# Kernel tuning notes

Hardware: AMD Instinct MI355X
Metric: run time of the kernel (lower is better)

## Reference

```python
import jax, jax.numpy as jnp
import numpy as np

DIMS = 1024
HEAD = 16
HEAD_DIM = DIMS // HEAD  # 64
BASE_THETA = 10000.0


def setup_inputs() -> dict:
    key = jax.random.key(0)
    ks = jax.random.split(key, 8)
    B, S = 2, 2048
    x = jax.random.normal(ks[0], (B, S, DIMS), dtype=jnp.float32)
    # causal additive mask (use -1e9 instead of -inf for finite grads)
    mask = jnp.where(jnp.tril(jnp.ones((S, S), dtype=bool)), 0.0, -1e9).astype(jnp.float32)
    init = 0.02
    Wq = jax.random.normal(ks[1], (DIMS, DIMS), dtype=jnp.float32) * init
    bq = jnp.zeros((DIMS,), dtype=jnp.float32)
    Wk = jax.random.normal(ks[2], (DIMS, DIMS), dtype=jnp.float32) * init  # no bias
    Wv = jax.random.normal(ks[3], (DIMS, DIMS), dtype=jnp.float32) * init
    bv = jnp.zeros((DIMS,), dtype=jnp.float32)
    Wo = jax.random.normal(ks[4], (DIMS, DIMS), dtype=jnp.float32) * init
    bo = jnp.zeros((DIMS,), dtype=jnp.float32)
    # learned rotary frequencies, initialized exactly as the torch module
    inv_freq = (1.0 / (BASE_THETA ** (jnp.arange(0, HEAD_DIM, 2, dtype=jnp.float32) / HEAD_DIM))).astype(jnp.float32)
    return {"x": x, "mask": mask, "Wq": Wq, "bq": bq, "Wk": Wk, "Wv": Wv,
            "bv": bv, "Wo": Wo, "bo": bo, "inv_freq": inv_freq}


def _apply_rotary(x, cos, sin):
    # x: [B,H,S,D] with D == 2 * len(inv_freq); cos/sin: [S, D/2]
    xr = x.reshape(*x.shape[:-1], -1, 2)  # [B,H,S,D/2,2]
    a, b = xr[..., 0], xr[..., 1]
    ra = a * cos - b * sin
    rb = a * sin + b * cos
    return jnp.stack([ra, rb], axis=-1).reshape(x.shape)


def reference(x, mask, Wq, bq, Wk, Wv, bv, Wo, bo, inv_freq):
    B, S, D = x.shape
    H, hd = HEAD, HEAD_DIM
    q = jnp.einsum('bsd,ed->bse', x, Wq) + bq
    k = jnp.einsum('bsd,ed->bse', x, Wk)
    v = jnp.einsum('bsd,ed->bse', x, Wv) + bv
    # [B,S,D] -> [B,H,S,hd]
    q = q.reshape(B, S, H, hd).transpose(0, 2, 1, 3)
    k = k.reshape(B, S, H, hd).transpose(0, 2, 1, 3)
    v = v.reshape(B, S, H, hd).transpose(0, 2, 1, 3)
    # rotary embeddings (complex mul expressed with cos/sin)
    t = jnp.arange(S, dtype=jnp.float32)
    freqs = t[:, None] * inv_freq[None, :]  # [S, hd/2]
    cos, sin = jnp.cos(freqs), jnp.sin(freqs)
    q = _apply_rotary(q, cos, sin)
    k = _apply_rotary(k, cos, sin)
    scale = hd ** (-0.25)
    qk = jnp.einsum('bhqd,bhkd->bhqk', q * scale, k * scale)
    qk = qk + mask[:S, :S]
    qk = qk.astype(jnp.float32)
    w = jax.nn.softmax(qk, axis=-1)  # dropout is identity in eval mode
    out = jnp.einsum('bhqk,bhkd->bhqd', w, v)
    out = out.transpose(0, 2, 1, 3).reshape(B, S, D)
    out = jnp.einsum('bsd,ed->bse', out, Wo) + bo
    return (out, qk)
```

## Files before the change

### kernel.cpp

```cpp
#include <hip/hip_runtime.h>

typedef __attribute__((ext_vector_type(8))) short short8;
typedef __attribute__((ext_vector_type(4))) float floatx4;
typedef unsigned short ushort_t;

typedef __attribute__((address_space(1))) const ushort_t gas_ushort;
typedef __attribute__((address_space(3))) ushort_t las_ushort;

static __device__ __forceinline__ ushort_t f2bf(float f) {
  union { float f; unsigned u; } v; v.f = f;
  unsigned r = v.u + 0x7fffu + ((v.u >> 16) & 1u);
  return (ushort_t)(r >> 16);
}
static __device__ __forceinline__ float bf2f(ushort_t s) {
  union { unsigned u; float f; } v; v.u = ((unsigned)s) << 16; return v.f;
}

#define L2E 1.4426950408889634f

__global__ void conv_kernel(const float* __restrict__ src, ushort_t* __restrict__ dst, int n) {
  int i = (blockIdx.x * blockDim.x + threadIdx.x) * 4;
  if (i >= n) return;
  float4 f = *(const float4*)(src + i);
  ushort4 u;
  u.x = f2bf(f.x); u.y = f2bf(f.y); u.z = f2bf(f.z); u.w = f2bf(f.w);
  *(ushort4*)(dst + i) = u;
}

__global__ void biascat_kernel(const float* __restrict__ bq, const float* __restrict__ bv,
                               float* __restrict__ bcat) {
  int i = blockIdx.x * blockDim.x + threadIdx.x;
  float v = 0.f;
  if (i < 1024) v = bq[i];
  else if (i >= 2048) v = bv[i - 2048];
  bcat[i] = v;
}

__global__ __launch_bounds__(256) void gemm_bt(
    const ushort_t* __restrict__ A, const ushort_t* __restrict__ Bm,
    const float* __restrict__ bias, float* __restrict__ Cf,
    ushort_t* __restrict__ Cb, int M, int N, int K)
{
  __shared__ ushort_t As[128 * 64];
  __shared__ ushort_t Bs[128 * 64];
  const int tid = threadIdx.x;
  const int wave = tid >> 6, lane = tid & 63;
  const int wm = wave >> 1, wn = wave & 1;
  const int lane15 = lane & 15, quad = lane >> 4;
  const int m0 = blockIdx.y * 128, n0 = blockIdx.x * 128;
  const int srow = lane >> 3;
  const int scol = (lane & 7) * 8;

  floatx4 acc[4][4];
#pragma unroll
  for (int a = 0; a < 4; ++a)
#pragma unroll
    for (int b = 0; b < 4; ++b) acc[a][b] = (floatx4){0.f, 0.f, 0.f, 0.f};

  for (int k0 = 0; k0 < K; k0 += 64) {
    __syncthreads();
#pragma unroll
    for (int pc = 0; pc < 4; ++pc) {
      const int chunk = pc * 4 + wave;
      const int row = chunk * 8 + srow;
      __builtin_amdgcn_global_load_lds(
          (gas_ushort*)(A + (size_t)(m0 + row) * K + k0 + scol),
          (las_ushort*)(As + chunk * 512 + lane * 8), 16, 0, 0);
      __builtin_amdgcn_global_load_lds(
          (gas_ushort*)(Bm + (size_t)(n0 + row) * K + k0 + scol),
          (las_ushort*)(Bs + chunk * 512 + lane * 8), 16, 0, 0);
    }
    __syncthreads();
#pragma unroll
    for (int ks = 0; ks < 64; ks += 32) {
      short8 af[4], bf[4];
#pragma unroll
      for (int mi = 0; mi < 4; ++mi)
        af[mi] = *(const short8*)(&As[(wm * 64 + mi * 16 + lane15) * 64 + ks + quad * 8]);
#pragma unroll
      for (int ni = 0; ni < 4; ++ni)
        bf[ni] = *(const short8*)(&Bs[(wn * 64 + ni * 16 + lane15) * 64 + ks + quad * 8]);
#pragma unroll
      for (int mi = 0; mi < 4; ++mi)
#pragma unroll
        for (int ni = 0; ni < 4; ++ni)
          acc[mi][ni] = __builtin_amdgcn_mfma_f32_16x16x32_bf16(af[mi], bf[ni], acc[mi][ni], 0, 0, 0);
    }
  }

#pragma unroll
  for (int mi = 0; mi < 4; ++mi) {
#pragma unroll
    for (int ni = 0; ni < 4; ++ni) {
      const int col = n0 + wn * 64 + ni * 16 + lane15;
      const float bv = bias ? bias[col] : 0.f;
#pragma unroll
      for (int v = 0; v < 4; ++v) {
        const int row = m0 + wm * 64 + mi * 16 + quad * 4 + v;
        const float val = acc[mi][ni][v] + bv;
        if (Cf) Cf[(size_t)row * N + col] = val;
        else    Cb[(size_t)row * N + col] = f2bf(val);
      }
    }
  }
}

__global__ void rotary_kernel(ushort_t* __restrict__ qkv, const float* __restrict__ inv_freq,
                              int colbase) {
  int tid = blockIdx.x * blockDim.x + threadIdx.x;
  int f = tid & 31;
  int h = (tid >> 5) & 15;
  int s = (tid >> 9) & 2047;
  int b = tid >> 20;
  size_t idx = (size_t)(b * 2048 + s) * 3072 + colbase + h * 64 + 2 * f;
  float ang = (float)s * inv_freq[f];
  float sn, cs;
  sincosf(ang, &sn, &cs);
  float a = bf2f(qkv[idx]);
  float bb = bf2f(qkv[idx + 1]);
  qkv[idx]     = f2bf(a * cs - bb * sn);
  qkv[idx + 1] = f2bf(a * sn + bb * cs);
}

__global__ void transpose_v_kernel(const ushort_t* __restrict__ QKV, ushort_t* __restrict__ VtG) {
  int g = blockIdx.x * blockDim.x + threadIdx.x;
  int s = g & 2047;
  int dchunk = (g >> 11) & 7;
  int bh = g >> 14;
  int b = bh >> 4, h = bh & 15;
  short8 v = *(const short8*)(QKV + (size_t)(b * 2048 + s) * 3072 + 2048 + h * 64 + dchunk * 8);
  ushort_t* dst = VtG + (size_t)bh * 64 * 2048 + (size_t)dchunk * 8 * 2048 + s;
#pragma unroll
  for (int e = 0; e < 8; ++e) dst[(size_t)e * 2048] = (ushort_t)v[e];
}

__global__ void fill_kernel(float* __restrict__ qk_out) {
  const int tile = blockIdx.x;
  const int it = tile >> 4, jt = tile & 15;
  if (jt <= it) return;
  const float4 val = {-1e9f, -1e9f, -1e9f, -1e9f};
  float* base = qk_out + (size_t)blockIdx.y * 2048 * 2048 + (size_t)it * 128 * 2048 + jt * 128;
#pragma unroll
  for (int l = 0; l < 16; ++l) {
    int idx = l * 256 + threadIdx.x;
    int row = idx >> 5, c4 = (idx & 31) * 4;
    *(float4*)(base + (size_t)row * 2048 + c4) = val;
  }
}

__global__ __launch_bounds__(256) void score_kernel(
    const ushort_t* __restrict__ QKV, float* __restrict__ qk_out,
    float2* __restrict__ pstats )
{
  const int tid = threadIdx.x;
  const int w = tid >> 6, lane = tid & 63;
  const int lane15 = lane & 15, quad = lane >> 4;
  const int t = blockIdx.x;
  const int bh = blockIdx.y;
  const int b = bh >> 4, h = bh & 15;

  int it = (int)((sqrtf((float)(8 * t + 1)) - 1.0f) * 0.5f);
  while ((it + 1) * (it + 2) / 2 <= t) ++it;
  while (it * (it + 1) / 2 > t) --it;
  const int jt = t - it * (it + 1) / 2;

  const int i_base = it * 128 + w * 32;
  const int j0 = jt * 128;
  const size_t srow0 = (size_t)b * 2048;

  short8 aq[2][2];
#pragma unroll
  for (int mi = 0; mi < 2; ++mi)
#pragma unroll
    for (int kb = 0; kb < 2; ++kb)
      aq[mi][kb] = *(const short8*)(QKV + (srow0 + i_base + mi * 16 + lane15) * 3072
                                    + h * 64 + kb * 32 + quad * 8);

  floatx4 s[2][8];
#pragma unroll
  for (int mi = 0; mi < 2; ++mi)
#pragma unroll
    for (int ni = 0; ni < 8; ++ni) s[mi][ni] = (floatx4){0.f, 0.f, 0.f, 0.f};
#pragma unroll
  for (int ni = 0; ni < 8; ++ni) {
#pragma unroll
    for (int kb = 0; kb < 2; ++kb) {
      short8 bk = *(const short8*)(QKV + (srow0 + j0 + ni * 16 + lane15) * 3072
                                   + 1024 + h * 64 + kb * 32 + quad * 8);
      s[0][ni] = __builtin_amdgcn_mfma_f32_16x16x32_bf16(aq[0][kb], bk, s[0][ni], 0, 0, 0);
      s[1][ni] = __builtin_amdgcn_mfma_f32_16x16x32_bf16(aq[1][kb], bk, s[1][ni], 0, 0, 0);
    }
  }

  float* qk_bh = qk_out + (size_t)bh * 2048 * 2048;

#pragma unroll
  for (int mi = 0; mi < 2; ++mi) {
#pragma unroll
    for (int ni = 0; ni < 8; ++ni) {
      const int j_g = j0 + ni * 16 + lane15;
#pragma unroll
      for (int v = 0; v < 4; ++v) {
        const int i_g = i_base + mi * 16 + quad * 4 + v;
        float val = s[mi][ni][v] * 0.125f + ((j_g <= i_g) ? 0.f : -1e9f);
        s[mi][ni][v] = val;
        qk_bh[(size_t)i_g * 2048 + j_g] = val;
      }
    }
  }

#pragma unroll
  for (int mi = 0; mi < 2; ++mi) {
#pragma unroll
    for (int v = 0; v < 4; ++v) {
      float mv = -3.0e38f;
#pragma unroll
      for (int ni = 0; ni < 8; ++ni) mv = fmaxf(mv, s[mi][ni][v]);
#pragma unroll
      for (int off = 1; off < 16; off <<= 1)
        mv = fmaxf(mv, __shfl_xor(mv, off));
      float ls = 0.f;
#pragma unroll
      for (int ni = 0; ni < 8; ++ni)
        ls += exp2f((s[mi][ni][v] - mv) * L2E);
#pragma unroll
      for (int off = 1; off < 16; off <<= 1)
        ls += __shfl_xor(ls, off);
      if (lane15 == 0) {
        const int i_g = i_base + mi * 16 + quad * 4 + v;
        pstats[(size_t)(bh * 2048 + i_g) * 16 + jt] = make_float2(mv, ls);
      }
    }
  }
}

__global__ void stats_kernel(const float2* __restrict__ pstats, float2* __restrict__ fstats) {
  int r = blockIdx.x * blockDim.x + threadIdx.x;
  int i = r & 2047;
  int nt = (i >> 7) + 1;
  const float2* p = pstats + (size_t)r * 16;
  float m = -3.0e38f;
  for (int t = 0; t < nt; ++t) m = fmaxf(m, p[t].x);
  float l = 0.f;
  for (int t = 0; t < nt; ++t) l += p[t].y * exp2f((p[t].x - m) * L2E);
  fstats[r] = make_float2(m, 1.f / l);
}

__global__ __launch_bounds__(256) void pv_kernel(
    const float* __restrict__ qk, const ushort_t* __restrict__ VtG,
    const float2* __restrict__ fstats, ushort_t* __restrict__ AO)
{
  __shared__ float cbuf[2][2][4][64][4];
  const int tid = threadIdx.x;
  const int w = tid >> 6, lane = tid & 63;
  const int lane15 = lane & 15, quad = lane >> 4;
  const int pib = w >> 1, sub = w & 1;
  const int pairId = blockIdx.x * 2 + pib;
  const int bh = pairId >> 6, p = pairId & 63;
  const int b = bh >> 4, h = bh & 15;

  const float* qk_bh = qk + (size_t)bh * 2048 * 2048;
  const ushort_t* Vt_bh = VtG + (size_t)bh * 64 * 2048;
  const float2* fs = fstats + (size_t)bh * 2048;

  floatx4 o[2][4];
#pragma unroll
  for (int half = 0; half < 2; ++half)
#pragma unroll
    for (int nd = 0; nd < 4; ++nd) o[half][nd] = (floatx4){0.f, 0.f, 0.f, 0.f};

#pragma unroll
  for (int half = 0; half < 2; ++half) {
    const int s16 = half ? (127 - p) : p;
    const int i0 = s16 * 16;
    const int njt = (s16 >> 3) + 1;
    const float mr = fs[i0 + lane15].x;

    for (int jt = sub; jt < njt; jt += 2) {
      const int j0 = jt * 128;
      const float* srow = qk_bh + (size_t)(i0 + lane15) * 2048 + j0 + quad * 8;

      short8 ap[4];
#pragma unroll
      for (int kb = 0; kb < 4; ++kb) {
        float4 a0 = *(const float4*)(srow + kb * 32);
        float4 a1 = *(const float4*)(srow + kb * 32 + 4);
        short8 a;
        a[0] = (short)f2bf(exp2f((a0.x - mr) * L2E));
        a[1] = (short)f2bf(exp2f((a0.y - mr) * L2E));
        a[2] = (short)f2bf(exp2f((a0.z - mr) * L2E));
        a[3] = (short)f2bf(exp2f((a0.w - mr) * L2E));
        a[4] = (short)f2bf(exp2f((a1.x - mr) * L2E));
        a[5] = (short)f2bf(exp2f((a1.y - mr) * L2E));
        a[6] = (short)f2bf(exp2f((a1.z - mr) * L2E));
        a[7] = (short)f2bf(exp2f((a1.w - mr) * L2E));
        ap[kb] = a;
      }

#pragma unroll
      for (int kb = 0; kb < 4; ++kb)
#pragma unroll
        for (int nd = 0; nd < 4; ++nd) {
          short8 bv = *(const short8*)(Vt_bh + (size_t)(nd * 16 + lane15) * 2048
                                       + j0 + kb * 32 + quad * 8);
          o[half][nd] = __builtin_amdgcn_mfma_f32_16x16x32_bf16(ap[kb], bv, o[half][nd], 0, 0, 0);
        }
    }
  }

  if (sub == 1) {
#pragma unroll
    for (int half = 0; half < 2; ++half)
#pragma unroll
      for (int nd = 0; nd < 4; ++nd)
        *(floatx4*)&cbuf[pib][half][nd][lane][0] = o[half][nd];
  }
  __syncthreads();
  if (sub == 0) {
#pragma unroll
    for (int half = 0; half < 2; ++half) {
      const int s16 = half ? (127 - p) : p;
      const int i0 = s16 * 16;
      float inv[4];
#pragma unroll
      for (int v = 0; v < 4; ++v) inv[v] = fs[i0 + quad * 4 + v].y;
#pragma unroll
      for (int nd = 0; nd < 4; ++nd) {
        floatx4 t = *(const floatx4*)&cbuf[pib][half][nd][lane][0];
#pragma unroll
        for (int v = 0; v < 4; ++v) {
          const int i_g = i0 + quad * 4 + v;
          AO[((size_t)b * 2048 + i_g) * 1024 + h * 64 + nd * 16 + lane15] =
              f2bf((o[half][nd][v] + t[v]) * inv[v]);
        }
      }
    }
  }
}

extern "C" void kernel_launch(void* const* d_in, const int* in_sizes, int n_in,
                              void* d_out, int out_size, void* d_ws, size_t ws_size,
                              hipStream_t stream) {
  const float* x  = (const float*)d_in[0];
  const float* Wq = (const float*)d_in[2];
  const float* bq = (const float*)d_in[3];
  const float* Wk = (const float*)d_in[4];
  const float* Wv = (const float*)d_in[5];
  const float* bv = (const float*)d_in[6];
  const float* Wo = (const float*)d_in[7];
  const float* bo = (const float*)d_in[8];
  const float* inv_freq = (const float*)d_in[9];

  char* ws = (char*)d_ws;
  ushort_t* xb   = (ushort_t*)(ws);
  ushort_t* vtg  = (ushort_t*)(ws);
  ushort_t* wb   = (ushort_t*)(ws + ((size_t)8  << 20));
  float*    bcat = (float*)   (ws + ((size_t)16 << 20));
  float2*   fstats = (float2*)(ws + ((size_t)16 << 20));
  ushort_t* qkv  = (ushort_t*)(ws + ((size_t)17 << 20));
  float2*   pstats = (float2*)(ws + ((size_t)41 << 20));
  ushort_t* aob  = (ushort_t*)(ws + ((size_t)41 << 20));

  float* out0  = (float*)d_out;
  float* qkout = out0 + 4194304;

  conv_kernel<<<4096, 256, 0, stream>>>(x, xb, 4194304);
  conv_kernel<<<1024, 256, 0, stream>>>(Wq, wb,           1048576);
  conv_kernel<<<1024, 256, 0, stream>>>(Wk, wb + 1048576, 1048576);
  conv_kernel<<<1024, 256, 0, stream>>>(Wv, wb + 2097152, 1048576);
  conv_kernel<<<1024, 256, 0, stream>>>(Wo, wb + 3145728, 1048576);
  biascat_kernel<<<12, 256, 0, stream>>>(bq, bv, bcat);

  gemm_bt<<<dim3(24, 32), 256, 0, stream>>>(xb, wb, bcat, nullptr, qkv, 4096, 3072, 1024);

  rotary_kernel<<<8192, 256, 0, stream>>>(qkv, inv_freq, 0);
  rotary_kernel<<<8192, 256, 0, stream>>>(qkv, inv_freq, 1024);

  transpose_v_kernel<<<2048, 256, 0, stream>>>(qkv, vtg);

  fill_kernel<<<dim3(256, 32), 256, 0, stream>>>(qkout);

  score_kernel<<<dim3(136, 32), 256, 0, stream>>>(qkv, qkout, pstats);

  stats_kernel<<<256, 256, 0, stream>>>(pstats, fstats);

  pv_kernel<<<1024, 256, 0, stream>>>(qkout, vtg, fstats, aob);

  gemm_bt<<<dim3(8, 32), 256, 0, stream>>>(aob, wb + 3145728, bo, out0, nullptr, 4096, 1024, 1024);
}
```

Before: 927.6 us.

## Fuse mask fill into score kernel, tile V transpose, split PV across four waves

The separate fill kernel is folded into the score kernel. The score kernel now launches a full 16x16 tile grid, in reverse row order, and upper-triangle blocks write -1e9 with nontemporal stores. The V transpose goes through shared memory so that both its reads and writes are coalesced. The PV kernel now gives each row-pair block to four waves, each taking every fourth key tile. It prefetches the next tile of scores into registers and folds the max subtraction into an FMA. Partial results are reduced through LDS, at the cost of more registers and extra barriers.

```diff
diff --git a/kernel.cpp b/kernel.cpp
--- a/kernel.cpp
+++ b/kernel.cpp
@@ -122,29 +122,30 @@
   qkv[idx + 1] = f2bf(a * sn + bb * cs);
 }
 
-__global__ void transpose_v_kernel(const ushort_t* __restrict__ QKV, ushort_t* __restrict__ VtG) {
-  int g = blockIdx.x * blockDim.x + threadIdx.x;
-  int s = g & 2047;
-  int dchunk = (g >> 11) & 7;
-  int bh = g >> 14;
-  int b = bh >> 4, h = bh & 15;
-  short8 v = *(const short8*)(QKV + (size_t)(b * 2048 + s) * 3072 + 2048 + h * 64 + dchunk * 8);
-  ushort_t* dst = VtG + (size_t)bh * 64 * 2048 + (size_t)dchunk * 8 * 2048 + s;
-#pragma unroll
-  for (int e = 0; e < 8; ++e) dst[(size_t)e * 2048] = (ushort_t)v[e];
-}
-
-__global__ void fill_kernel(float* __restrict__ qk_out) {
-  const int tile = blockIdx.x;
-  const int it = tile >> 4, jt = tile & 15;
-  if (jt <= it) return;
-  const float4 val = {-1e9f, -1e9f, -1e9f, -1e9f};
-  float* base = qk_out + (size_t)blockIdx.y * 2048 * 2048 + (size_t)it * 128 * 2048 + jt * 128;
-#pragma unroll
-  for (int l = 0; l < 16; ++l) {
-    int idx = l * 256 + threadIdx.x;
-    int row = idx >> 5, c4 = (idx & 31) * 4;
-    *(float4*)(base + (size_t)row * 2048 + c4) = val;
+__global__ __launch_bounds__(256) void transpose_v_kernel(
+    const ushort_t* __restrict__ QKV, ushort_t* __restrict__ VtG) {
+  __shared__ ushort_t T[32][74];
+  const int tid = threadIdx.x;
+  const int st = blockIdx.x;
+  const int bh = blockIdx.y;
+  const int b = bh >> 4, h = bh & 15;
+
+  {
+    const int s_l = tid >> 3;
+    const int d0 = (tid & 7) * 8;
+    short8 v = *(const short8*)(QKV + (size_t)(b * 2048 + st * 32 + s_l) * 3072
+                                + 2048 + h * 64 + d0);
+#pragma unroll
+    for (int e = 0; e < 8; ++e) T[s_l][d0 + e] = (ushort_t)v[e];
+  }
+  __syncthreads();
+  {
+    const int d_l = tid >> 2;
+    const int s0 = (tid & 3) * 8;
+    short8 v;
+#pragma unroll
+    for (int e = 0; e < 8; ++e) v[e] = (short)T[s0 + e][d_l];
+    *(short8*)(VtG + (size_t)bh * 131072 + (size_t)d_l * 2048 + st * 32 + s0) = v;
   }
 }
 
@@ -153,17 +154,26 @@
     float2* __restrict__ pstats )
 {
   const int tid = threadIdx.x;
+  const int it = 15 - (blockIdx.x >> 4);
+  const int jt = blockIdx.x & 15;
+  const int bh = blockIdx.y;
+  float* qk_bh = qk_out + (size_t)bh * 2048 * 2048;
+
+  if (jt > it) {
+    const floatx4 val = {-1e9f, -1e9f, -1e9f, -1e9f};
+    float* base = qk_bh + (size_t)it * 128 * 2048 + jt * 128;
+#pragma unroll
+    for (int l = 0; l < 16; ++l) {
+      int idx = l * 256 + tid;
+      int row = idx >> 5, c4 = (idx & 31) * 4;
+      __builtin_nontemporal_store(val, (floatx4*)(base + (size_t)row * 2048 + c4));
+    }
+    return;
+  }
+
   const int w = tid >> 6, lane = tid & 63;
   const int lane15 = lane & 15, quad = lane >> 4;
-  const int t = blockIdx.x;
-  const int bh = blockIdx.y;
   const int b = bh >> 4, h = bh & 15;
-
-  int it = (int)((sqrtf((float)(8 * t + 1)) - 1.0f) * 0.5f);
-  while ((it + 1) * (it + 2) / 2 <= t) ++it;
-  while (it * (it + 1) / 2 > t) --it;
-  const int jt = t - it * (it + 1) / 2;
-
   const int i_base = it * 128 + w * 32;
   const int j0 = jt * 128;
   const size_t srow0 = (size_t)b * 2048;
@@ -191,8 +201,6 @@
       s[1][ni] = __builtin_amdgcn_mfma_f32_16x16x32_bf16(aq[1][kb], bk, s[1][ni], 0, 0, 0);
     }
   }
-
-  float* qk_bh = qk_out + (size_t)bh * 2048 * 2048;
 
 #pragma unroll
   for (int mi = 0; mi < 2; ++mi) {
@@ -250,91 +258,102 @@
     const float* __restrict__ qk, const ushort_t* __restrict__ VtG,
     const float2* __restrict__ fstats, ushort_t* __restrict__ AO)
 {
-  __shared__ float cbuf[2][2][4][64][4];
+  __shared__ float cbuf[3][4][64][4];
   const int tid = threadIdx.x;
   const int w = tid >> 6, lane = tid & 63;
   const int lane15 = lane & 15, quad = lane >> 4;
-  const int pib = w >> 1, sub = w & 1;
-  const int pairId = blockIdx.x * 2 + pib;
+  const int pairId = blockIdx.x;
   const int bh = pairId >> 6, p = pairId & 63;
   const int b = bh >> 4, h = bh & 15;
 
   const float* qk_bh = qk + (size_t)bh * 2048 * 2048;
-  const ushort_t* Vt_bh = VtG + (size_t)bh * 64 * 2048;
+  const ushort_t* Vt_bh = VtG + (size_t)bh * 131072;
   const float2* fs = fstats + (size_t)bh * 2048;
 
-  floatx4 o[2][4];
-#pragma unroll
-  for (int half = 0; half < 2; ++half)
-#pragma unroll
-    for (int nd = 0; nd < 4; ++nd) o[half][nd] = (floatx4){0.f, 0.f, 0.f, 0.f};
-
-#pragma unroll
   for (int half = 0; half < 2; ++half) {
     const int s16 = half ? (127 - p) : p;
     const int i0 = s16 * 16;
     const int njt = (s16 >> 3) + 1;
     const float mr = fs[i0 + lane15].x;
-
-    for (int jt = sub; jt < njt; jt += 2) {
+    const float mrl = mr * L2E;
+    const float* srow = qk_bh + (size_t)(i0 + lane15) * 2048 + quad * 8;
+
+    floatx4 o[4];
+#pragma unroll
+    for (int nd = 0; nd < 4; ++nd) o[nd] = (floatx4){0.f, 0.f, 0.f, 0.f};
+
+    floatx4 curA[8];
+    if (w < njt) {
+#pragma unroll
+      for (int c = 0; c < 8; ++c)
+        curA[c] = *(const floatx4*)(srow + w * 128 + (c >> 1) * 32 + (c & 1) * 4);
+    }
+
+    for (int jt = w; jt < njt; jt += 4) {
+      const int jn = jt + 4;
+      floatx4 nxtA[8];
+      if (jn < njt) {
+#pragma unroll
+        for (int c = 0; c < 8; ++c)
+          nxtA[c] = *(const floatx4*)(srow + jn * 128 + (c >> 1) * 32 + (c & 1) * 4);
+      }
+
+      short8 ap[4];
+#pragma unroll
+      for (int kb = 0; kb < 4; ++kb) {
+        floatx4 a0 = curA[kb * 2], a1 = curA[kb * 2 + 1];
+        short8 a;
+        a[0] = (short)f2bf(exp2f(__builtin_fmaf(a0.x, L2E, -mrl)));
+        a[1] = (short)f2bf(exp2f(__builtin_fmaf(a0.y, L2E, -mrl)));
+        a[2] = (short)f2bf(exp2f(__builtin_fmaf(a0.z, L2E, -mrl)));
+        a[3] = (short)f2bf(exp2f(__builtin_fmaf(a0.w, L2E, -mrl)));
+        a[4] = (short)f2bf(exp2f(__builtin_fmaf(a1.x, L2E, -mrl)));
+        a[5] = (short)f2bf(exp2f(__builtin_fmaf(a1.y, L2E, -mrl)));
+        a[6] = (short)f2bf(exp2f(__builtin_fmaf(a1.z, L2E, -mrl)));
+        a[7] = (short)f2bf(exp2f(__builtin_fmaf(a1.w, L2E, -mrl)));
+        ap[kb] = a;
+      }
+
       const int j0 = jt * 128;
-      const float* srow = qk_bh + (size_t)(i0 + lane15) * 2048 + j0 + quad * 8;
-
-      short8 ap[4];
-#pragma unroll
-      for (int kb = 0; kb < 4; ++kb) {
-        float4 a0 = *(const float4*)(srow + kb * 32);
-        float4 a1 = *(const float4*)(srow + kb * 32 + 4);
-        short8 a;
-        a[0] = (short)f2bf(exp2f((a0.x - mr) * L2E));
-        a[1] = (short)f2bf(exp2f((a0.y - mr) * L2E));
-        a[2] = (short)f2bf(exp2f((a0.z - mr) * L2E));
-        a[3] = (short)f2bf(exp2f((a0.w - mr) * L2E));
-        a[4] = (short)f2bf(exp2f((a1.x - mr) * L2E));
-        a[5] = (short)f2bf(exp2f((a1.y - mr) * L2E));
-        a[6] = (short)f2bf(exp2f((a1.z - mr) * L2E));
-        a[7] = (short)f2bf(exp2f((a1.w - mr) * L2E));
-        ap[kb] = a;
-      }
-
 #pragma unroll
       for (int kb = 0; kb < 4; ++kb)
 #pragma unroll
         for (int nd = 0; nd < 4; ++nd) {
           short8 bv = *(const short8*)(Vt_bh + (size_t)(nd * 16 + lane15) * 2048
                                        + j0 + kb * 32 + quad * 8);
-          o[half][nd] = __builtin_amdgcn_mfma_f32_16x16x32_bf16(ap[kb], bv, o[half][nd], 0, 0, 0);
+          o[nd] = __builtin_amdgcn_mfma_f32_16x16x32_bf16(ap[kb], bv, o[nd], 0, 0, 0);
         }
-    }
-  }
-
-  if (sub == 1) {
-#pragma unroll
-    for (int half = 0; half < 2; ++half)
+
+      if (jn < njt) {
+#pragma unroll
+        for (int c = 0; c < 8; ++c) curA[c] = nxtA[c];
+      }
+    }
+
+    if (w) {
 #pragma unroll
       for (int nd = 0; nd < 4; ++nd)
-        *(floatx4*)&cbuf[pib][half][nd][lane][0] = o[half][nd];
-  }
-  __syncthreads();
-  if (sub == 0) {
-#pragma unroll
-    for (int half = 0; half < 2; ++half) {
-      const int s16 = half ? (127 - p) : p;
-      const int i0 = s16 * 16;
+        *(floatx4*)&cbuf[w - 1][nd][lane][0] = o[nd];
+    }
+    __syncthreads();
+    if (w == 0) {
       float inv[4];
 #pragma unroll
       for (int v = 0; v < 4; ++v) inv[v] = fs[i0 + quad * 4 + v].y;
 #pragma unroll
       for (int nd = 0; nd < 4; ++nd) {
-        floatx4 t = *(const floatx4*)&cbuf[pib][half][nd][lane][0];
+        floatx4 t = o[nd];
+#pragma unroll
+        for (int sl = 0; sl < 3; ++sl) t += *(const floatx4*)&cbuf[sl][nd][lane][0];
 #pragma unroll
         for (int v = 0; v < 4; ++v) {
           const int i_g = i0 + quad * 4 + v;
           AO[((size_t)b * 2048 + i_g) * 1024 + h * 64 + nd * 16 + lane15] =
-              f2bf((o[half][nd][v] + t[v]) * inv[v]);
+              f2bf(t[v] * inv[v]);
         }
       }
     }
+    __syncthreads();
   }
 }
 
@@ -376,15 +395,13 @@
   rotary_kernel<<<8192, 256, 0, stream>>>(qkv, inv_freq, 0);
   rotary_kernel<<<8192, 256, 0, stream>>>(qkv, inv_freq, 1024);
 
-  transpose_v_kernel<<<2048, 256, 0, stream>>>(qkv, vtg);
-
-  fill_kernel<<<dim3(256, 32), 256, 0, stream>>>(qkout);
-
-  score_kernel<<<dim3(136, 32), 256, 0, stream>>>(qkv, qkout, pstats);
+  transpose_v_kernel<<<dim3(64, 32), 256, 0, stream>>>(qkv, vtg);
+
+  score_kernel<<<dim3(256, 32), 256, 0, stream>>>(qkv, qkout, pstats);
 
   stats_kernel<<<256, 256, 0, stream>>>(pstats, fstats);
 
-  pv_kernel<<<1024, 256, 0, stream>>>(qkout, vtg, fstats, aob);
+  pv_kernel<<<2048, 256, 0, stream>>>(qkout, vtg, fstats, aob);
 
   gemm_bt<<<dim3(8, 32), 256, 0, stream>>>(aob, wb + 3145728, bo, out0, nullptr, 4096, 1024, 1024);
 }
```

After: 878.7 us. -5.3%, faster.
